# Kernel optimization log

Hardware: AMD Instinct MI355X
Metric: run time of the kernel (lower is better)

The kernel has to match this reference:

```python
import jax, jax.numpy as jnp
import numpy as np

B, T, C, H = 4, 2048, 768, 12
D = C // H  # head dim = 64
EPS = 1e-5


def setup_inputs() -> dict:
    key = jax.random.key(0)
    ks = jax.random.split(key, 12)
    s = lambda fan_in: 1.0 / np.sqrt(fan_in)
    return {
        "x": jax.random.normal(ks[0], (B, T, C), dtype=jnp.float32),
        "ln1_g": jnp.ones((C,), jnp.float32),
        "ln1_b": jnp.zeros((C,), jnp.float32),
        "w_attn": jax.random.normal(ks[1], (C, 3 * C), jnp.float32) * s(C),
        "b_attn": jnp.zeros((3 * C,), jnp.float32),
        "w_aproj": jax.random.normal(ks[2], (C, C), jnp.float32) * s(C),
        "b_aproj": jnp.zeros((C,), jnp.float32),
        "ln2_g": jnp.ones((C,), jnp.float32),
        "ln2_b": jnp.zeros((C,), jnp.float32),
        "w_fc": jax.random.normal(ks[3], (C, 4 * C), jnp.float32) * s(C),
        "b_fc": jnp.zeros((4 * C,), jnp.float32),
        "w_mproj": jax.random.normal(ks[4], (4 * C, C), jnp.float32) * s(4 * C),
        "b_mproj": jnp.zeros((C,), jnp.float32),
    }


def _layernorm(x, g, b):
    mu = jnp.mean(x, axis=-1, keepdims=True)
    var = jnp.mean(jnp.square(x - mu), axis=-1, keepdims=True)
    return (x - mu) * jax.lax.rsqrt(var + EPS) * g + b


def _attention(h, w_attn, b_attn, w_aproj, b_aproj):
    qkv = h @ w_attn + b_attn                          # [B,T,3C]
    q, k, v = jnp.split(qkv, 3, axis=-1)
    q = q.reshape(B, T, H, D)
    k = k.reshape(B, T, H, D)
    v = v.reshape(B, T, H, D)
    att = jnp.einsum("bqhd,bkhd->bhqk", q, k) * (1.0 / np.sqrt(D))
    causal = jnp.tril(jnp.ones((T, T), bool))
    att = jnp.where(causal, att, -jnp.inf)
    att = jax.nn.softmax(att, axis=-1)
    y = jnp.einsum("bhqk,bkhd->bqhd", att, v).reshape(B, T, C)
    return y @ w_aproj + b_aproj


def reference(x, ln1_g, ln1_b, w_attn, b_attn, w_aproj, b_aproj,
              ln2_g, ln2_b, w_fc, b_fc, w_mproj, b_mproj):
    x = x + _attention(_layernorm(x, ln1_g, ln1_b), w_attn, b_attn, w_aproj, b_aproj)
    h = _layernorm(x, ln2_g, ln2_b)
    h = jax.nn.gelu(h @ w_fc + b_fc, approximate=True)  # tanh approximation, matches F.gelu(approximate='tanh')
    x = x + (h @ w_mproj + b_mproj)
    return x
```

## Files before the change

### kernel.cpp

```cpp
#include <hip/hip_runtime.h>


typedef unsigned short ushortT;
typedef unsigned int uintT;
typedef __attribute__((ext_vector_type(8))) __bf16 bf16x8;
typedef __attribute__((ext_vector_type(4))) float f32x4;

#define MFMA16(a, b, c) __builtin_amdgcn_mfma_f32_16x16x32_bf16(a, b, c, 0, 0, 0)

__device__ inline float b2f(ushortT u) {
  return __uint_as_float(((uintT)u) << 16);
}
__device__ inline ushortT f2b(float f) {
  uintT x = __float_as_uint(f);
  uintT r = x + 0x7fffu + ((x >> 16) & 1u);
  return (ushortT)(r >> 16);
}
__device__ inline uintT pack_bf2(float a, float b) {
  return __builtin_amdgcn_perm(__float_as_uint(b), __float_as_uint(a),
                               0x07060302u);
}

__device__ inline float fast_exp2(float x) {
#if __has_builtin(__builtin_amdgcn_exp2f)
  return __builtin_amdgcn_exp2f(x);
#else
  return exp2f(x);
#endif
}

__device__ inline float gelu_tanh(float v) {
  float t = 0.7978845608028654f * (v + 0.044715f * v * v * v);
  return v / (1.0f + __expf(-2.0f * t));
}

__device__ __forceinline__ void glds16(const ushortT* g, ushortT* l) {
  __builtin_amdgcn_global_load_lds(
      (const __attribute__((address_space(1))) unsigned int*)(const void*)g,
      (__attribute__((address_space(3))) unsigned int*)(void*)l, 16, 0, 0);
}

__global__ __launch_bounds__(256) void detect_dtype(
    const ushortT* __restrict__ w, int* __restrict__ flag) {
  __shared__ int red;
  if (threadIdx.x == 0) red = 0;
  __syncthreads();
  int crazy = 0;
  for (int i = threadIdx.x; i < 4096; i += 256) {
    uintT e = (w[2 * i] >> 7) & 0xFF;
    if (e >= 150) crazy = 1;
  }
  if (crazy) atomicOr(&red, 1);
  __syncthreads();
  if (threadIdx.x == 0) *flag = red;
}

struct VecArgs {
  const void* src[8];
  int n[8];
  int dstoff[8];
};
__global__ __launch_bounds__(256) void convert_vecs(
    VecArgs a, ushortT* __restrict__ pv, const int* __restrict__ flag) {
  int fl = *flag;
  int t = blockIdx.y;
  int i = blockIdx.x * 256 + threadIdx.x;
  if (i >= a.n[t]) return;
  float v = fl ? ((const float*)a.src[t])[i] : b2f(((const ushortT*)a.src[t])[i]);
  pv[a.dstoff[t] + i] = f2b(v);
}

__global__ __launch_bounds__(256) void transpose_any(
    const void* __restrict__ in, ushortT* __restrict__ out, int K, int N,
    const int* __restrict__ flag) {
  __shared__ ushortT t[32][33];
  int fl = *flag;
  int n0 = blockIdx.x * 32, k0 = blockIdx.y * 32;
  int x = threadIdx.x, y0 = threadIdx.y;
#pragma unroll
  for (int i = y0; i < 32; i += 8) {
    size_t idx = (size_t)(k0 + i) * N + n0 + x;
    t[i][x] = fl ? f2b(((const float*)in)[idx]) : ((const ushortT*)in)[idx];
  }
  __syncthreads();
#pragma unroll
  for (int i = y0; i < 32; i += 8)
    out[(size_t)(n0 + i) * K + k0 + x] = t[x][i];
}

__global__ __launch_bounds__(256) void vtrans_kernel(
    const ushortT* __restrict__ qkv, ushortT* __restrict__ vt) {
  const int T = 2048, C3 = 2304;
  __shared__ ushortT tile[64][65];
  int bh = blockIdx.y;
  int b = bh / 12, h = bh % 12;
  int t0 = blockIdx.x * 64;
  int col = threadIdx.x & 63, rowi = threadIdx.x >> 6;
#pragma unroll
  for (int rr = rowi; rr < 64; rr += 4)
    tile[rr][col] =
        qkv[((size_t)(b * T + t0 + rr)) * C3 + 1536 + h * 64 + col];
  __syncthreads();
#pragma unroll
  for (int dd = rowi; dd < 64; dd += 4)
    vt[((size_t)bh * 64 + dd) * T + t0 + col] = tile[col][dd];
}

template <int MODE>
__global__ __launch_bounds__(256) void ln_kernel(
    const void* __restrict__ xin, const ushortT* __restrict__ g,
    const ushortT* __restrict__ bb, ushortT* __restrict__ out,
    const int* __restrict__ flag) {
  const int C = 768;
  bool f32;
  if constexpr (MODE == 1) f32 = true; else f32 = (*flag != 0);
  size_t base = (size_t)blockIdx.x * C;
  int tid = threadIdx.x;
  const float* xf = (const float*)xin;
  const ushortT* xb = (const ushortT*)xin;
  float v0 = f32 ? xf[base + tid]       : b2f(xb[base + tid]);
  float v1 = f32 ? xf[base + tid + 256] : b2f(xb[base + tid + 256]);
  float v2 = f32 ? xf[base + tid + 512] : b2f(xb[base + tid + 512]);
  float s = v0 + v1 + v2;
  float q = v0 * v0 + v1 * v1 + v2 * v2;
#pragma unroll
  for (int off = 32; off; off >>= 1) {
    s += __shfl_xor(s, off);
    q += __shfl_xor(q, off);
  }
  __shared__ float as_[4], aq_[4];
  if ((tid & 63) == 0) { as_[tid >> 6] = s; aq_[tid >> 6] = q; }
  __syncthreads();
  s = as_[0] + as_[1] + as_[2] + as_[3];
  q = aq_[0] + aq_[1] + aq_[2] + aq_[3];
  float mu = s * (1.0f / 768.0f);
  float var = q * (1.0f / 768.0f) - mu * mu;
  float rs = rsqrtf(var + 1e-5f);
  ushortT* orow = out + base;
  orow[tid]       = f2b((v0 - mu) * rs * b2f(g[tid])       + b2f(bb[tid]));
  orow[tid + 256] = f2b((v1 - mu) * rs * b2f(g[tid + 256]) + b2f(bb[tid + 256]));
  orow[tid + 512] = f2b((v2 - mu) * rs * b2f(g[tid + 512]) + b2f(bb[tid + 512]));
}

template <int EPI>
__global__ __launch_bounds__(512, 2) void gemm_dp(
    const ushortT* __restrict__ A, const ushortT* __restrict__ Bt,
    const ushortT* __restrict__ bias, const void* __restrict__ res,
    void* __restrict__ out, int N, int K, int nbm, int nbn,
    const int* __restrict__ flag) {
  __shared__ ushortT As3[3][128 * 64];
  __shared__ ushortT Bs3[3][256 * 64];
  int fl = (EPI >= 2) ? *flag : 0;
  int tid = threadIdx.x;
  int lane = tid & 63, wave = tid >> 6;
  int quad = lane >> 4, n = lane & 15, n7 = n & 7;
  int mg = wave >> 2, ng = wave & 3;
  int l = blockIdx.x;
  int xcd = l & 7, j = l >> 3;
  int m0 = (xcd * (nbm >> 3) + j / nbn) * 128;
  int n0 = (j % nbn) * 256;

  int trow = tid >> 3;
  int tc = ((tid & 7) ^ (trow & 7)) << 3;
  const ushortT* ga = A + (size_t)(m0 + trow) * K + tc;
  const ushortT* gb = Bt + (size_t)(n0 + trow) * K + tc;
  int lw = wave * 512;

  const int c0 = (quad ^ n7) << 3;
  const int c1 = ((4 + quad) ^ n7) << 3;
  const int arow = (mg * 64 + n) * 64;
  const int brow = (ng * 64 + n) * 64;

  int kt = K >> 6;
  f32x4 acc[4][4] = {};

  auto stage_tile = [&](int tt, int slot) {
    int kk0 = tt << 6;
    ushortT* la = &As3[slot][0] + lw;
    ushortT* lb = &Bs3[slot][0] + lw;
    glds16(ga + kk0, la);
    glds16(ga + (size_t)64 * K + kk0, la + 4096);
    glds16(gb + kk0, lb);
    glds16(gb + (size_t)64 * K + kk0, lb + 4096);
    glds16(gb + (size_t)128 * K + kk0, lb + 8192);
    glds16(gb + (size_t)192 * K + kk0, lb + 12288);
  };

  stage_tile(0, 0);
  stage_tile(1, 1);
  asm volatile("s_waitcnt vmcnt(6)" ::: "memory");
  __builtin_amdgcn_s_barrier();

  int cur = 0;
  for (int t = 0; t < kt; ++t) {
    const ushortT* ca = &As3[cur][0];
    const ushortT* cb = &Bs3[cur][0];
    int nxt = cur + 2; if (nxt >= 3) nxt -= 3;
    bool pf = (t + 2) < kt;
    int pk0 = (t + 2) << 6;
    ushortT* la = &As3[nxt][0] + lw;
    ushortT* lb = &Bs3[nxt][0] + lw;

    bf16x8 af[4][2], bfr[2][2];
#pragma unroll
    for (int mi = 0; mi < 4; ++mi) {
      af[mi][0] = *(const bf16x8*)(ca + arow + mi * 1024 + c0);
      af[mi][1] = *(const bf16x8*)(ca + arow + mi * 1024 + c1);
    }
#pragma unroll
    for (int ni = 0; ni < 2; ++ni) {
      bfr[ni][0] = *(const bf16x8*)(cb + brow + ni * 1024 + c0);
      bfr[ni][1] = *(const bf16x8*)(cb + brow + ni * 1024 + c1);
    }
    if (pf) {
      glds16(ga + pk0, la);
      glds16(ga + (size_t)64 * K + pk0, la + 4096);
      glds16(gb + pk0, lb);
    }
    __builtin_amdgcn_s_barrier();
    __builtin_amdgcn_s_setprio(1);
#pragma unroll
    for (int mi = 0; mi < 4; ++mi)
#pragma unroll
      for (int ni = 0; ni < 2; ++ni) {
        acc[mi][ni] = MFMA16(af[mi][0], bfr[ni][0], acc[mi][ni]);
        acc[mi][ni] = MFMA16(af[mi][1], bfr[ni][1], acc[mi][ni]);
      }
    __builtin_amdgcn_s_setprio(0);
    __builtin_amdgcn_s_barrier();

#pragma unroll
    for (int ni = 0; ni < 2; ++ni) {
      bfr[ni][0] = *(const bf16x8*)(cb + brow + (ni + 2) * 1024 + c0);
      bfr[ni][1] = *(const bf16x8*)(cb + brow + (ni + 2) * 1024 + c1);
    }
    if (pf) {
      glds16(gb + (size_t)64 * K + pk0, lb + 4096);
      glds16(gb + (size_t)128 * K + pk0, lb + 8192);
      glds16(gb + (size_t)192 * K + pk0, lb + 12288);
    }
    __builtin_amdgcn_s_barrier();
    __builtin_amdgcn_s_setprio(1);
#pragma unroll
    for (int mi = 0; mi < 4; ++mi)
#pragma unroll
      for (int ni = 0; ni < 2; ++ni) {
        acc[mi][ni + 2] = MFMA16(af[mi][0], bfr[ni][0], acc[mi][ni + 2]);
        acc[mi][ni + 2] = MFMA16(af[mi][1], bfr[ni][1], acc[mi][ni + 2]);
      }
    __builtin_amdgcn_s_setprio(0);
    if (pf) asm volatile("s_waitcnt vmcnt(6)" ::: "memory");
    else    asm volatile("s_waitcnt vmcnt(0)" ::: "memory");
    __builtin_amdgcn_s_barrier();

    cur = cur + 1; if (cur == 3) cur = 0;
  }

#pragma unroll
  for (int mi = 0; mi < 4; ++mi) {
#pragma unroll
    for (int ni = 0; ni < 4; ++ni) {
      int gc = n0 + ng * 64 + ni * 16 + n;
      float bv = b2f(bias[gc]);
      int gr0 = m0 + mg * 64 + mi * 16 + quad * 4;
#pragma unroll
      for (int r = 0; r < 4; ++r) {
        size_t idx = (size_t)(gr0 + r) * N + gc;
        float v = acc[mi][ni][r] + bv;
        if constexpr (EPI == 1) v = gelu_tanh(v);
        if constexpr (EPI == 2) {
          v += fl ? ((const float*)res)[idx] : b2f(((const ushortT*)res)[idx]);
          ((float*)out)[idx] = v;
        } else if constexpr (EPI == 3) {
          v += ((const float*)res)[idx];
          if (fl) ((float*)out)[idx] = v;
          else    ((ushortT*)out)[idx] = f2b(v);
        } else {
          ((ushortT*)out)[idx] = f2b(v);
        }
      }
    }
  }
}

__global__ __launch_bounds__(256) void attn_kernel(
    const ushortT* __restrict__ qkv, const ushortT* __restrict__ vt,
    ushortT* __restrict__ y) {
  const int T = 2048, C3 = 2304;
  constexpr int LDP = 72;
  __shared__ ushortT Ks[2][64 * 64];
  __shared__ ushortT Vs[2][64 * 64];
  __shared__ ushortT Ps[4 * 16 * LDP];
  int bh = blockIdx.y;
  int b = bh / 12, h = bh % 12;
  int pj = blockIdx.x;
  int tid = threadIdx.x;
  int lane = tid & 63, wave = tid >> 6;
  int quad = lane >> 4, n = lane & 15, n7 = n & 7;

  const ushortT* base = qkv + (size_t)b * T * C3;
  const ushortT* kbase = base + 768 + h * 64;
  const ushortT* vbase = vt + (size_t)bh * 64 * T;
  ushortT* myP = Ps + wave * 16 * LDP;

  const float QS = 0.18033688011112042f;
  const float MB = 20.0f;

  int qtA = pj, qtB = 31 - pj;
  int nA = qtA + 1, ntot = 33;

  int srow = lane >> 3, scol = lane & 7;
  const ushortT* kg =
      kbase + (size_t)(wave * 16 + srow) * C3 + ((scol ^ srow) << 3);
  const ushortT* vg =
      vbase + (size_t)(wave * 16 + srow) * T + ((scol ^ srow) << 3);

  const int c0 = (quad ^ n7) << 3;
  const int c1 = ((4 + quad) ^ n7) << 3;

  int qt = qtA;
  int qw = qt * 64 + wave * 16;
  bf16x8 aq[2];
  {
    const ushortT* qrow = base + (size_t)(qw + n) * C3 + h * 64 + quad * 8;
#pragma unroll
    for (int dh = 0; dh < 2; ++dh) {
      union { ushortT u[8]; bf16x8 v; } tmp;
#pragma unroll
      for (int j = 0; j < 8; ++j) tmp.u[j] = f2b(b2f(qrow[dh * 32 + j]) * QS);
      aq[dh] = tmp.v;
    }
  }
  f32x4 Ot[4] = {};
  float l_ = 0.f;

  auto stage = [&](int kt_, int buf) {
    int kof = kt_ << 6;
    ushortT* lk = &Ks[buf][0] + wave * 1024;
    ushortT* lv = &Vs[buf][0] + wave * 1024;
    glds16(kg + (size_t)kof * C3, lk);
    glds16(kg + (size_t)(kof + 8) * C3, lk + 512);
    glds16(vg + kof, lv);
    glds16(vg + (size_t)8 * T + kof, lv + 512);
  };

  stage(0, 0);
  __syncthreads();

  int cur = 0;
  for (int t = 0; t < ntot; ++t) {
    int kt = (t < nA) ? t : t - nA;
    if (t + 1 < ntot) {
      int ktn = (t + 1 < nA) ? t + 1 : t + 1 - nA;
      stage(ktn, cur ^ 1);
    }
    const ushortT* ks = &Ks[cur][0];
    const ushortT* vs = &Vs[cur][0];

    f32x4 St[4];
#pragma unroll
    for (int g = 0; g < 4; ++g) {
      bf16x8 ka0 = *(const bf16x8*)(ks + (g * 16 + n) * 64 + c0);
      bf16x8 ka1 = *(const bf16x8*)(ks + (g * 16 + n) * 64 + c1);
      f32x4 z = {};
      z = MFMA16(ka0, aq[0], z);
      St[g] = MFMA16(ka1, aq[1], z);
    }
    if (kt == qt) {
      int lim = wave * 16 + n;
#pragma unroll
      for (int g = 0; g < 4; ++g)
#pragma unroll
        for (int r = 0; r < 4; ++r)
          if (g * 16 + quad * 4 + r > lim) St[g][r] = -1e30f;
    }
    float ls = 0.f;
#pragma unroll
    for (int g = 0; g < 4; ++g) {
      float p0 = fast_exp2(St[g][0] - MB);
      float p1 = fast_exp2(St[g][1] - MB);
      float p2 = fast_exp2(St[g][2] - MB);
      float p3 = fast_exp2(St[g][3] - MB);
      ls += (p0 + p1) + (p2 + p3);
      uint2 pk;
      pk.x = pack_bf2(p0, p1);
      pk.y = pack_bf2(p2, p3);
      *(uint2*)(myP + n * LDP + g * 16 + quad * 4) = pk;
    }
    ls += __shfl_xor(ls, 16);
    ls += __shfl_xor(ls, 32);
    l_ += ls;

    bf16x8 pb0 = *(const bf16x8*)(myP + n * LDP + quad * 8);
    bf16x8 pb1 = *(const bf16x8*)(myP + n * LDP + 32 + quad * 8);
#pragma unroll
    for (int dt = 0; dt < 4; ++dt) {
      bf16x8 va0 = *(const bf16x8*)(vs + (dt * 16 + n) * 64 + c0);
      bf16x8 va1 = *(const bf16x8*)(vs + (dt * 16 + n) * 64 + c1);
      Ot[dt] = MFMA16(va0, pb0, Ot[dt]);
      Ot[dt] = MFMA16(va1, pb1, Ot[dt]);
    }

    if (kt == qt) {
      float inv = 1.0f / l_;
      int qg = qw + n;
#pragma unroll
      for (int dt = 0; dt < 4; ++dt) {
        uint2 o;
        o.x = pack_bf2(Ot[dt][0] * inv, Ot[dt][1] * inv);
        o.y = pack_bf2(Ot[dt][2] * inv, Ot[dt][3] * inv);
        *(uint2*)(y + (size_t)(b * T + qg) * 768 + h * 64 + dt * 16 +
                  quad * 4) = o;
      }
      if (t + 1 < ntot) {
        qt = qtB;
        qw = qt * 64 + wave * 16;
        const ushortT* qrow =
            base + (size_t)(qw + n) * C3 + h * 64 + quad * 8;
#pragma unroll
        for (int dh = 0; dh < 2; ++dh) {
          union { ushortT u[8]; bf16x8 v; } tmp;
#pragma unroll
          for (int j = 0; j < 8; ++j)
            tmp.u[j] = f2b(b2f(qrow[dh * 32 + j]) * QS);
          aq[dh] = tmp.v;
        }
#pragma unroll
        for (int dt = 0; dt < 4; ++dt)
#pragma unroll
          for (int r = 0; r < 4; ++r) Ot[dt][r] = 0.f;
        l_ = 0.f;
      }
    }
    __syncthreads();
    cur ^= 1;
  }
}

extern "C" void kernel_launch(void* const* d_in, const int* in_sizes, int n_in,
                              void* d_out, int out_size, void* d_ws,
                              size_t ws_size, hipStream_t stream) {
  (void)in_sizes; (void)n_in; (void)out_size; (void)ws_size;
  const void* x       = d_in[0];
  const void* w_attn  = d_in[3];
  const void* w_aproj = d_in[5];
  const void* w_fc    = d_in[9];
  const void* w_mproj = d_in[11];

  char* ws = (char*)d_ws;
  ushortT* h1  = (ushortT*)(ws);
  ushortT* qkv = (ushortT*)(ws + 12582912);
  ushortT* yb  = (ushortT*)(ws + 50331648);
  float*   x1  = (float*)(ws + 62914560);
  ushortT* fcg = (ushortT*)(ws + 88080384);
  ushortT* wT0 = (ushortT*)(ws + 138412032);
  ushortT* wT1 = (ushortT*)(ws + 141950976);
  ushortT* wT2 = (ushortT*)(ws + 143130624);
  ushortT* wT3 = (ushortT*)(ws + 147849216);
  ushortT* pv  = (ushortT*)(ws + 152567808);
  int*     flag = (int*)(ws + 152600576);
  ushortT* vt  = h1;
  ushortT* h2  = yb;

  const int O_LN1G = 0, O_LN1B = 768, O_BATT = 1536, O_BAPR = 3840,
            O_LN2G = 4608, O_LN2B = 5376, O_BFC = 6144, O_BMPR = 9216;

  detect_dtype<<<1, 256, 0, stream>>>((const ushortT*)w_fc, flag);

  VecArgs va;
  va.src[0] = d_in[1];  va.n[0] = 768;  va.dstoff[0] = O_LN1G;
  va.src[1] = d_in[2];  va.n[1] = 768;  va.dstoff[1] = O_LN1B;
  va.src[2] = d_in[4];  va.n[2] = 2304; va.dstoff[2] = O_BATT;
  va.src[3] = d_in[6];  va.n[3] = 768;  va.dstoff[3] = O_BAPR;
  va.src[4] = d_in[7];  va.n[4] = 768;  va.dstoff[4] = O_LN2G;
  va.src[5] = d_in[8];  va.n[5] = 768;  va.dstoff[5] = O_LN2B;
  va.src[6] = d_in[10]; va.n[6] = 3072; va.dstoff[6] = O_BFC;
  va.src[7] = d_in[12]; va.n[7] = 768;  va.dstoff[7] = O_BMPR;
  convert_vecs<<<dim3(12, 8), 256, 0, stream>>>(va, pv, flag);

  dim3 tb(32, 8);
  transpose_any<<<dim3(72, 24), tb, 0, stream>>>(w_attn, wT0, 768, 2304, flag);
  transpose_any<<<dim3(24, 24), tb, 0, stream>>>(w_aproj, wT1, 768, 768, flag);
  transpose_any<<<dim3(96, 24), tb, 0, stream>>>(w_fc, wT2, 768, 3072, flag);
  transpose_any<<<dim3(24, 96), tb, 0, stream>>>(w_mproj, wT3, 3072, 768, flag);

  ln_kernel<0><<<8192, 256, 0, stream>>>(x, pv + O_LN1G, pv + O_LN1B, h1, flag);
  gemm_dp<0><<<576, 512, 0, stream>>>(
      h1, wT0, pv + O_BATT, nullptr, qkv, 2304, 768, 64, 9, flag);
  vtrans_kernel<<<dim3(32, 48), 256, 0, stream>>>(qkv, vt);
  attn_kernel<<<dim3(16, 48), 256, 0, stream>>>(qkv, vt, yb);
  gemm_dp<2><<<192, 512, 0, stream>>>(
      yb, wT1, pv + O_BAPR, x, x1, 768, 768, 64, 3, flag);
  ln_kernel<1><<<8192, 256, 0, stream>>>(x1, pv + O_LN2G, pv + O_LN2B, h2, flag);
  gemm_dp<1><<<768, 512, 0, stream>>>(
      h2, wT2, pv + O_BFC, nullptr, fcg, 3072, 768, 64, 12, flag);
  gemm_dp<3><<<192, 512, 0, stream>>>(
      fcg, wT3, pv + O_BMPR, x1, d_out, 768, 3072, 64, 3, flag);
}
```

Measured before the change: 421.9 us.

## Replace triple-buffered 128x256 GEMM with simple single-buffer 128x128 GEMM

Swaps the 512-thread, triple-buffered, phase-interleaved GEMM kernel for a 256-thread kernel using 128x128 tiles, one LDS buffer and a plain sync-load-sync-compute loop. Grid sizes double to cover the smaller tiles. This lowers LDS use and per-block size, which can raise occupancy and the number of blocks. In exchange it drops the software prefetch overlap, so global loads are no longer hidden behind the MFMA work.

```diff
diff --git a/kernel.cpp b/kernel.cpp
--- a/kernel.cpp
+++ b/kernel.cpp
@@ -143,126 +143,73 @@
 }
 
 template <int EPI>
-__global__ __launch_bounds__(512, 2) void gemm_dp(
+__global__ __launch_bounds__(256) void gemm_sb(
     const ushortT* __restrict__ A, const ushortT* __restrict__ Bt,
     const ushortT* __restrict__ bias, const void* __restrict__ res,
     void* __restrict__ out, int N, int K, int nbm, int nbn,
     const int* __restrict__ flag) {
-  __shared__ ushortT As3[3][128 * 64];
-  __shared__ ushortT Bs3[3][256 * 64];
+  __shared__ ushortT As[128 * 64];
+  __shared__ ushortT Bs[128 * 64];
   int fl = (EPI >= 2) ? *flag : 0;
   int tid = threadIdx.x;
   int lane = tid & 63, wave = tid >> 6;
   int quad = lane >> 4, n = lane & 15, n7 = n & 7;
-  int mg = wave >> 2, ng = wave & 3;
+  int wm = (wave >> 1) * 64, wn = (wave & 1) * 64;
   int l = blockIdx.x;
   int xcd = l & 7, j = l >> 3;
   int m0 = (xcd * (nbm >> 3) + j / nbn) * 128;
-  int n0 = (j % nbn) * 256;
+  int n0 = (j % nbn) * 128;
 
   int trow = tid >> 3;
   int tc = ((tid & 7) ^ (trow & 7)) << 3;
   const ushortT* ga = A + (size_t)(m0 + trow) * K + tc;
   const ushortT* gb = Bt + (size_t)(n0 + trow) * K + tc;
-  int lw = wave * 512;
+  const int ldst = wave * 512;
 
   const int c0 = (quad ^ n7) << 3;
   const int c1 = ((4 + quad) ^ n7) << 3;
-  const int arow = (mg * 64 + n) * 64;
-  const int brow = (ng * 64 + n) * 64;
-
-  int kt = K >> 6;
+  const int arow = (wm + n) * 64;
+  const int brow = (wn + n) * 64;
+
   f32x4 acc[4][4] = {};
 
-  auto stage_tile = [&](int tt, int slot) {
-    int kk0 = tt << 6;
-    ushortT* la = &As3[slot][0] + lw;
-    ushortT* lb = &Bs3[slot][0] + lw;
-    glds16(ga + kk0, la);
-    glds16(ga + (size_t)64 * K + kk0, la + 4096);
-    glds16(gb + kk0, lb);
-    glds16(gb + (size_t)64 * K + kk0, lb + 4096);
-    glds16(gb + (size_t)128 * K + kk0, lb + 8192);
-    glds16(gb + (size_t)192 * K + kk0, lb + 12288);
-  };
-
-  stage_tile(0, 0);
-  stage_tile(1, 1);
-  asm volatile("s_waitcnt vmcnt(6)" ::: "memory");
-  __builtin_amdgcn_s_barrier();
-
-  int cur = 0;
-  for (int t = 0; t < kt; ++t) {
-    const ushortT* ca = &As3[cur][0];
-    const ushortT* cb = &Bs3[cur][0];
-    int nxt = cur + 2; if (nxt >= 3) nxt -= 3;
-    bool pf = (t + 2) < kt;
-    int pk0 = (t + 2) << 6;
-    ushortT* la = &As3[nxt][0] + lw;
-    ushortT* lb = &Bs3[nxt][0] + lw;
-
-    bf16x8 af[4][2], bfr[2][2];
+  for (int k0 = 0; k0 < K; k0 += 64) {
+    __syncthreads();
+#pragma unroll
+    for (int i = 0; i < 4; ++i)
+      glds16(ga + (size_t)(i * 32) * K + k0, As + ldst + i * 2048);
+#pragma unroll
+    for (int i = 0; i < 4; ++i)
+      glds16(gb + (size_t)(i * 32) * K + k0, Bs + ldst + i * 2048);
+    __syncthreads();
+
+    bf16x8 af[4][2], bfr[4][2];
 #pragma unroll
     for (int mi = 0; mi < 4; ++mi) {
-      af[mi][0] = *(const bf16x8*)(ca + arow + mi * 1024 + c0);
-      af[mi][1] = *(const bf16x8*)(ca + arow + mi * 1024 + c1);
-    }
-#pragma unroll
-    for (int ni = 0; ni < 2; ++ni) {
-      bfr[ni][0] = *(const bf16x8*)(cb + brow + ni * 1024 + c0);
-      bfr[ni][1] = *(const bf16x8*)(cb + brow + ni * 1024 + c1);
-    }
-    if (pf) {
-      glds16(ga + pk0, la);
-      glds16(ga + (size_t)64 * K + pk0, la + 4096);
-      glds16(gb + pk0, lb);
-    }
-    __builtin_amdgcn_s_barrier();
-    __builtin_amdgcn_s_setprio(1);
+      af[mi][0] = *(const bf16x8*)(As + arow + mi * 1024 + c0);
+      af[mi][1] = *(const bf16x8*)(As + arow + mi * 1024 + c1);
+    }
+#pragma unroll
+    for (int ni = 0; ni < 4; ++ni) {
+      bfr[ni][0] = *(const bf16x8*)(Bs + brow + ni * 1024 + c0);
+      bfr[ni][1] = *(const bf16x8*)(Bs + brow + ni * 1024 + c1);
+    }
 #pragma unroll
     for (int mi = 0; mi < 4; ++mi)
 #pragma unroll
-      for (int ni = 0; ni < 2; ++ni) {
+      for (int ni = 0; ni < 4; ++ni) {
         acc[mi][ni] = MFMA16(af[mi][0], bfr[ni][0], acc[mi][ni]);
         acc[mi][ni] = MFMA16(af[mi][1], bfr[ni][1], acc[mi][ni]);
       }
-    __builtin_amdgcn_s_setprio(0);
-    __builtin_amdgcn_s_barrier();
-
-#pragma unroll
-    for (int ni = 0; ni < 2; ++ni) {
-      bfr[ni][0] = *(const bf16x8*)(cb + brow + (ni + 2) * 1024 + c0);
-      bfr[ni][1] = *(const bf16x8*)(cb + brow + (ni + 2) * 1024 + c1);
-    }
-    if (pf) {
-      glds16(gb + (size_t)64 * K + pk0, lb + 4096);
-      glds16(gb + (size_t)128 * K + pk0, lb + 8192);
-      glds16(gb + (size_t)192 * K + pk0, lb + 12288);
-    }
-    __builtin_amdgcn_s_barrier();
-    __builtin_amdgcn_s_setprio(1);
-#pragma unroll
-    for (int mi = 0; mi < 4; ++mi)
-#pragma unroll
-      for (int ni = 0; ni < 2; ++ni) {
-        acc[mi][ni + 2] = MFMA16(af[mi][0], bfr[ni][0], acc[mi][ni + 2]);
-        acc[mi][ni + 2] = MFMA16(af[mi][1], bfr[ni][1], acc[mi][ni + 2]);
-      }
-    __builtin_amdgcn_s_setprio(0);
-    if (pf) asm volatile("s_waitcnt vmcnt(6)" ::: "memory");
-    else    asm volatile("s_waitcnt vmcnt(0)" ::: "memory");
-    __builtin_amdgcn_s_barrier();
-
-    cur = cur + 1; if (cur == 3) cur = 0;
   }
 
 #pragma unroll
   for (int mi = 0; mi < 4; ++mi) {
 #pragma unroll
     for (int ni = 0; ni < 4; ++ni) {
-      int gc = n0 + ng * 64 + ni * 16 + n;
+      int gc = n0 + wn + ni * 16 + n;
       float bv = b2f(bias[gc]);
-      int gr0 = m0 + mg * 64 + mi * 16 + quad * 4;
+      int gr0 = m0 + wm + mi * 16 + quad * 4;
 #pragma unroll
       for (int r = 0; r < 4; ++r) {
         size_t idx = (size_t)(gr0 + r) * N + gc;
@@ -485,15 +432,15 @@
   transpose_any<<<dim3(24, 96), tb, 0, stream>>>(w_mproj, wT3, 3072, 768, flag);
 
   ln_kernel<0><<<8192, 256, 0, stream>>>(x, pv + O_LN1G, pv + O_LN1B, h1, flag);
-  gemm_dp<0><<<576, 512, 0, stream>>>(
-      h1, wT0, pv + O_BATT, nullptr, qkv, 2304, 768, 64, 9, flag);
+  gemm_sb<0><<<1152, 256, 0, stream>>>(
+      h1, wT0, pv + O_BATT, nullptr, qkv, 2304, 768, 64, 18, flag);
   vtrans_kernel<<<dim3(32, 48), 256, 0, stream>>>(qkv, vt);
   attn_kernel<<<dim3(16, 48), 256, 0, stream>>>(qkv, vt, yb);
-  gemm_dp<2><<<192, 512, 0, stream>>>(
-      yb, wT1, pv + O_BAPR, x, x1, 768, 768, 64, 3, flag);
+  gemm_sb<2><<<384, 256, 0, stream>>>(
+      yb, wT1, pv + O_BAPR, x, x1, 768, 768, 64, 6, flag);
   ln_kernel<1><<<8192, 256, 0, stream>>>(x1, pv + O_LN2G, pv + O_LN2B, h2, flag);
-  gemm_dp<1><<<768, 512, 0, stream>>>(
-      h2, wT2, pv + O_BFC, nullptr, fcg, 3072, 768, 64, 12, flag);
-  gemm_dp<3><<<192, 512, 0, stream>>>(
-      fcg, wT3, pv + O_BMPR, x1, d_out, 768, 3072, 64, 3, flag);
-}
+  gemm_sb<1><<<1536, 256, 0, stream>>>(
+      h2, wT2, pv + O_BFC, nullptr, fcg, 3072, 768, 64, 24, flag);
+  gemm_sb<3><<<384, 256, 0, stream>>>(
+      fcg, wT3, pv + O_BMPR, x1, d_out, 768, 3072, 64, 6, flag);
+}
```

After: 438.0 us. 1.04x slower.
